# Kernel optimization log

Measured on AMD Instinct MI355X. Metric: run time of the kernel, lower is better.

Reference implementation:

```python
import jax, jax.numpy as jnp
import numpy as np

SOS_TOKEN = 0
VOCAB, EMBED, HIDDEN = 32000, 256, 256


def setup_inputs() -> dict:
    key = jax.random.key(0)
    ks = jax.random.split(key, 10)
    B, S, T = 32, 128, 128
    s = 0.05
    return {
        "encoder_outputs": jax.random.normal(ks[0], (B, S, HIDDEN), jnp.float32),
        "encoder_hidden": jax.random.normal(ks[1], (1, B, HIDDEN), jnp.float32),
        "target_tensor": jax.random.randint(ks[2], (B, T), 0, VOCAB),
        "embedding": jax.random.normal(ks[3], (VOCAB, EMBED), jnp.float32) * s,
        "W_ih": jax.random.normal(ks[4], (3 * HIDDEN, EMBED + HIDDEN), jnp.float32) * s,
        "W_hh": jax.random.normal(ks[5], (3 * HIDDEN, HIDDEN), jnp.float32) * s,
        "b_ih": jax.random.normal(ks[6], (3 * HIDDEN,), jnp.float32) * s,
        "b_hh": jax.random.normal(ks[7], (3 * HIDDEN,), jnp.float32) * s,
        "W_out": jax.random.normal(ks[8], (VOCAB, HIDDEN), jnp.float32) * s,
        "b_out": jax.random.normal(ks[9], (VOCAB,), jnp.float32) * s,
    }


def _decode(encoder_outputs, encoder_hidden, target_tensor, embedding,
            W_ih, W_hh, b_ih, b_hh, W_out, b_out):
    B, T = target_tensor.shape
    # full teacher forcing: decoder input at step t is target[t-1], step 0 is SOS
    dec_in = jnp.concatenate(
        [jnp.full((B, 1), SOS_TOKEN, dtype=target_tensor.dtype), target_tensor[:, :-1]], axis=1)
    emb = embedding[dec_in]                                     # (B,T,E)
    # attention: query = embedded input, key = value = encoder_outputs
    scores = jnp.einsum("bte,bse->bts", emb, encoder_outputs)   # (B,T,S)
    attn = jax.nn.softmax(scores, axis=2)
    context = jnp.einsum("bts,bsh->bth", attn, encoder_outputs)  # (B,T,H)
    x_seq = jnp.concatenate([emb, context], axis=2)             # (B,T,E+H)
    x_seq = jnp.swapaxes(x_seq, 0, 1)                           # (T,B,E+H)

    def gru_step(h, x):
        gi = x @ W_ih.T + b_ih                                  # (B,3H)
        gh = h @ W_hh.T + b_hh
        i_r, i_z, i_n = jnp.split(gi, 3, axis=1)
        h_r, h_z, h_n = jnp.split(gh, 3, axis=1)
        r = jax.nn.sigmoid(i_r + h_r)
        z = jax.nn.sigmoid(i_z + h_z)
        n = jnp.tanh(i_n + r * h_n)
        h_new = (1.0 - z) * n + z * h
        return h_new, h_new

    h0 = encoder_hidden[0]                                      # (B,H)
    _, hs = jax.lax.scan(gru_step, h0, x_seq)                   # (T,B,H)
    logits = hs @ W_out.T + b_out                               # (T,B,V)
    return jnp.swapaxes(logits, 0, 1)                           # (B,T,V)


def reference(encoder_outputs, encoder_hidden, target_tensor, embedding,
              W_ih, W_hh, b_ih, b_hh, W_out, b_out):
    return _decode(encoder_outputs, encoder_hidden, target_tensor, embedding,
                   W_ih, W_hh, b_ih, b_hh, W_out, b_out)
```

## Files before the change

### kernel.cpp

```cpp
#include <hip/hip_runtime.h>
#include <hip/hip_bf16.h>
#include <stdint.h>

typedef float    f32x4  __attribute__((ext_vector_type(4)));
typedef __bf16   bf16x8 __attribute__((ext_vector_type(8)));
typedef _Float16 f16x8  __attribute__((ext_vector_type(8)));
typedef _Float16 h2v    __attribute__((ext_vector_type(2)));

#define B_ 32
#define S_ 128
#define T_ 128
#define H_ 256
#define E_ 256
#define V_ 32000

__device__ __forceinline__ void gll16(const void* g, void* l) {
  __builtin_amdgcn_global_load_lds(
      (const __attribute__((address_space(1))) uint32_t*)g,
      (__attribute__((address_space(3))) uint32_t*)l,
      16, 0, 0);
}

__device__ __forceinline__ uint32_t pack_pair(float a, float b) {
  unsigned short lo = __builtin_bit_cast(unsigned short, (_Float16)a);
  unsigned short hi = __builtin_bit_cast(unsigned short, (_Float16)b);
  return (uint32_t)lo | ((uint32_t)hi << 16);
}

__device__ __forceinline__ uint32_t pack_bf16(float a, float b) {
  return (uint32_t)__builtin_bit_cast(unsigned short, __float2bfloat16(a)) |
         ((uint32_t)__builtin_bit_cast(unsigned short, __float2bfloat16(b)) << 16);
}

__device__ __forceinline__ float dot2(uint32_t w, uint32_t h, float acc) {
#if __has_builtin(__builtin_amdgcn_fdot2)
  return __builtin_amdgcn_fdot2(__builtin_bit_cast(h2v, w),
                                __builtin_bit_cast(h2v, h), acc, false);
#else
  h2v wv = __builtin_bit_cast(h2v, w);
  h2v hv = __builtin_bit_cast(h2v, h);
  return acc + (float)wv.x * (float)hv.x + (float)wv.y * (float)hv.y;
#endif
}

__device__ __forceinline__ float sigmoid_fast(float x) {
  return __fdividef(1.f, 1.f + __expf(-x));
}
__device__ __forceinline__ float tanh_fast(float x) {
  float e = __expf(2.f * fabsf(x));
  float t = 1.f - __fdividef(2.f, e + 1.f);
  return copysignf(t, x);
}

__global__ __launch_bounds__(256) void prep_kernel(
    const float* __restrict__ Wout, uint32_t* __restrict__ woutb,
    const float* __restrict__ Wih,  uint32_t* __restrict__ wihh,
    const float* __restrict__ Whh,  uint32_t* __restrict__ Wp,
    const float* __restrict__ enc, const int* __restrict__ tgt,
    const float* __restrict__ embt, uint32_t* __restrict__ xh)
{
  __shared__ __align__(16) char smem[32896];
  int bid = blockIdx.x;
  int tid = threadIdx.x;

  if (bid < 4000) {
    int i = (bid * 256 + tid) * 8;
    float4 a = *(const float4*)(Wout + i);
    float4 b = *(const float4*)(Wout + i + 4);
    uint4 o;
    o.x = pack_bf16(a.x, a.y); o.y = pack_bf16(a.z, a.w);
    o.z = pack_bf16(b.x, b.y); o.w = pack_bf16(b.z, b.w);
    *(uint4*)(woutb + (i >> 1)) = o;
    return;
  }
  if (bid < 4384) {
    int i = ((bid - 4000) * 256 + tid) * 4;
    float4 v = *(const float4*)(Wih + i);
    uint2 p;
    p.x = pack_pair(v.x, v.y);
    p.y = pack_pair(v.z, v.w);
    *(uint2*)(wihh + (i >> 1)) = p;
    return;
  }
  if (bid < 4408) {
    float (*lds)[257] = (float(*)[257])smem;
    int j0 = (bid - 4384) * 32;
    #pragma unroll 4
    for (int i = 0; i < 32; ++i)
      lds[i][tid] = Whh[(size_t)(j0 + i) * 256 + tid];
    __syncthreads();
    #pragma unroll 4
    for (int i = 0; i < 16; ++i) {
      int e = i * 256 + tid;
      int k2 = e >> 5;
      int jj = e & 31;
      Wp[(size_t)k2 * 768 + j0 + jj] = pack_pair(lds[jj][2 * k2], lds[jj][2 * k2 + 1]);
    }
    return;
  }
  {
    int idx = bid - 4408;
    int b   = idx & 31;
    int tc  = idx >> 5;
    float* e_sh    = (float*)smem;
    float* attn_sh = e_sh + 256;
    float* red_sh  = attn_sh + 128;
    const float* encb = enc + (size_t)b * S_ * H_;

    for (int tt = 0; tt < 8; ++tt) {
      int t = tc * 8 + tt;
      int tok = (t == 0) ? 0 : tgt[b * T_ + t - 1];
      float ev = embt[(size_t)tok * E_ + tid];
      e_sh[tid] = ev;
      {
        float other = __shfl_xor(ev, 1);
        if (!(tid & 1))
          xh[(size_t)(t * B_ + b) * 256 + (tid >> 1)] = pack_pair(ev, other);
      }
      __syncthreads();

      float sc = 0.f;
      if (tid < 128) {
        const float* er = encb + tid * H_;
        #pragma unroll 8
        for (int k = 0; k < 256; k += 4) {
          float4 e4 = *(const float4*)(e_sh + k);
          float4 r4 = *(const float4*)(er + k);
          sc += e4.x * r4.x; sc += e4.y * r4.y; sc += e4.z * r4.z; sc += e4.w * r4.w;
        }
        float mx = sc;
        #pragma unroll
        for (int o = 32; o > 0; o >>= 1) mx = fmaxf(mx, __shfl_xor(mx, o, 64));
        if ((tid & 63) == 0) red_sh[tid >> 6] = mx;
      }
      __syncthreads();
      float gmax = fmaxf(red_sh[0], red_sh[1]);
      float p = 0.f;
      if (tid < 128) {
        p = __expf(sc - gmax);
        float s = p;
        #pragma unroll
        for (int o = 32; o > 0; o >>= 1) s += __shfl_xor(s, o, 64);
        if ((tid & 63) == 0) red_sh[2 + (tid >> 6)] = s;
      }
      __syncthreads();
      float tot = red_sh[2] + red_sh[3];
      if (tid < 128) attn_sh[tid] = p / tot;
      __syncthreads();

      float ctx = 0.f;
      #pragma unroll 4
      for (int s = 0; s < 128; ++s) ctx += attn_sh[s] * encb[s * H_ + tid];
      {
        float other = __shfl_xor(ctx, 1);
        if (!(tid & 1))
          xh[(size_t)(t * B_ + b) * 256 + 128 + (tid >> 1)] = pack_pair(ctx, other);
      }
      __syncthreads();
    }
  }
}

__global__ __launch_bounds__(256) void gi_gemm_f16(
    const _Float16* __restrict__ A,
    const _Float16* __restrict__ Bm,
    const float* __restrict__ bih,
    float* __restrict__ gi)
{
  __shared__ _Float16 sA[128 * 64];
  __shared__ _Float16 sB[128 * 64];
  int tid = threadIdx.x;
  int n0 = blockIdx.x * 128;
  int m0 = blockIdx.y * 128;
  int lane = tid & 63;
  int wave = tid >> 6;
  int wm = (wave >> 1) * 64;
  int wn = (wave & 1) * 64;
  int srow = tid >> 3;
  int sk   = (tid & 7) * 8;
  f32x4 acc[4][4] = {};

  for (int kt = 0; kt < 512; kt += 64) {
    #pragma unroll
    for (int it = 0; it < 4; ++it) {
      int row = it * 32 + srow;
      gll16(A  + (size_t)(m0 + row) * 512 + kt + sk, &sA[row * 64 + sk]);
      gll16(Bm + (size_t)(n0 + row) * 512 + kt + sk, &sB[row * 64 + sk]);
    }
    __syncthreads();
    #pragma unroll
    for (int kk = 0; kk < 2; ++kk) {
      f16x8 af[4], bfr[4];
      #pragma unroll
      for (int m = 0; m < 4; ++m)
        af[m] = *(const f16x8*)&sA[(wm + m * 16 + (lane & 15)) * 64 + kk * 32 + (lane >> 4) * 8];
      #pragma unroll
      for (int n = 0; n < 4; ++n)
        bfr[n] = *(const f16x8*)&sB[(wn + n * 16 + (lane & 15)) * 64 + kk * 32 + (lane >> 4) * 8];
      #pragma unroll
      for (int m = 0; m < 4; ++m)
        #pragma unroll
        for (int n = 0; n < 4; ++n)
          acc[m][n] = __builtin_amdgcn_mfma_f32_16x16x32_f16(af[m], bfr[n], acc[m][n], 0, 0, 0);
    }
    __syncthreads();
  }

  #pragma unroll
  for (int n = 0; n < 4; ++n) {
    int col = n0 + wn + n * 16 + (lane & 15);
    float bv = bih[col];
    #pragma unroll
    for (int m = 0; m < 4; ++m) {
      int rbase = m0 + wm + m * 16 + (lane >> 4) * 4;
      #pragma unroll
      for (int r = 0; r < 4; ++r)
        gi[(size_t)(rbase + r) * 768 + col] = acc[m][n][r] + bv;
    }
  }
}

__global__ __launch_bounds__(768) void gru_kernel(
    const float*    __restrict__ gi,
    const uint32_t* __restrict__ Wp,
    const float*    __restrict__ bhh,
    const float*    __restrict__ h0,
    __hip_bfloat16* __restrict__ hs)
{
  int b   = blockIdx.x;
  int tid = threadIdx.x;
  int role = tid >> 8;
  int j    = tid & 255;
  __shared__ __align__(16) uint32_t h2[128];
  __shared__ float r_sh[256];
  __shared__ float z_sh[256];

  uint32_t w[128];
  #pragma unroll
  for (int i = 0; i < 128; ++i) w[i] = Wp[(size_t)i * 768 + tid];
  float bj = bhh[tid];

  float hprev = 0.f;
  if (role == 2) {
    hprev = h0[b * 256 + j];
    float other = __shfl_xor(hprev, 1);
    if (!(j & 1)) h2[j >> 1] = pack_pair(hprev, other);
  }
  float gval = gi[(size_t)b * 768 + tid];
  __syncthreads();

  for (int t = 0; t < 128; ++t) {
    float gnext = 0.f;
    if (t < 127) gnext = gi[(size_t)((t + 1) * 32 + b) * 768 + tid];

    float a0 = 0.f, a1 = 0.f, a2 = 0.f, a3 = 0.f;
    float a4 = 0.f, a5 = 0.f, a6 = 0.f, a7 = 0.f;
    #pragma unroll
    for (int k8 = 0; k8 < 16; ++k8) {
      uint4 ha = *(const uint4*)&h2[k8 * 8];
      uint4 hb = *(const uint4*)&h2[k8 * 8 + 4];
      a0 = dot2(w[k8 * 8 + 0], ha.x, a0);
      a1 = dot2(w[k8 * 8 + 1], ha.y, a1);
      a2 = dot2(w[k8 * 8 + 2], ha.z, a2);
      a3 = dot2(w[k8 * 8 + 3], ha.w, a3);
      a4 = dot2(w[k8 * 8 + 4], hb.x, a4);
      a5 = dot2(w[k8 * 8 + 5], hb.y, a5);
      a6 = dot2(w[k8 * 8 + 6], hb.z, a6);
      a7 = dot2(w[k8 * 8 + 7], hb.w, a7);
    }
    float gh = ((a0 + a1) + (a2 + a3)) + ((a4 + a5) + (a6 + a7)) + bj;

    if (role == 0)      r_sh[j] = sigmoid_fast(gval + gh);
    else if (role == 1) z_sh[j] = sigmoid_fast(gval + gh);
    __syncthreads();

    if (role == 2) {
      float r = r_sh[j];
      float z = z_sh[j];
      float n = tanh_fast(gval + r * gh);
      float hn = (1.f - z) * n + z * hprev;
      hprev = hn;
      hs[(size_t)(t * 32 + b) * 256 + j] = __float2bfloat16(hn);
      float other = __shfl_xor(hn, 1);
      if (!(j & 1)) h2[j >> 1] = pack_pair(hn, other);
    }
    gval = gnext;
    __syncthreads();
  }
}

__global__ __launch_bounds__(512) void logits_gemm(
    const __hip_bfloat16* __restrict__ A,
    const __hip_bfloat16* __restrict__ Bm,
    const float* __restrict__ bout,
    float* __restrict__ out)
{
  __shared__ __hip_bfloat16 sA[128 * 64];
  __shared__ __hip_bfloat16 sB[256 * 64];
  int tid = threadIdx.x;
  int bid = blockIdx.x;
  int chunk = bid & 7;
  int local = bid >> 3;
  int m0 = (chunk * 4 + (local & 3)) * 128;
  int n0 = (local >> 2) * 256;
  int lane = tid & 63;
  int wave = tid >> 6;
  int wm = (wave >> 2) * 64;
  int wn = (wave & 3) * 64;
  int srow = tid >> 3;
  int sk   = (tid & 7) * 8;
  f32x4 acc[4][4] = {};

  for (int kt = 0; kt < 256; kt += 64) {
    #pragma unroll
    for (int it = 0; it < 2; ++it) {
      int row = it * 64 + srow;
      gll16(A + (size_t)(m0 + row) * 256 + kt + sk, &sA[row * 64 + sk]);
    }
    #pragma unroll
    for (int it = 0; it < 4; ++it) {
      int row = it * 64 + srow;
      gll16(Bm + (size_t)(n0 + row) * 256 + kt + sk, &sB[row * 64 + sk]);
    }
    __syncthreads();
    #pragma unroll
    for (int kk = 0; kk < 2; ++kk) {
      bf16x8 af[4], bfr[4];
      #pragma unroll
      for (int m = 0; m < 4; ++m)
        af[m] = *(const bf16x8*)&sA[(wm + m * 16 + (lane & 15)) * 64 + kk * 32 + (lane >> 4) * 8];
      #pragma unroll
      for (int n = 0; n < 4; ++n)
        bfr[n] = *(const bf16x8*)&sB[(wn + n * 16 + (lane & 15)) * 64 + kk * 32 + (lane >> 4) * 8];
      #pragma unroll
      for (int m = 0; m < 4; ++m)
        #pragma unroll
        for (int n = 0; n < 4; ++n)
          acc[m][n] = __builtin_amdgcn_mfma_f32_16x16x32_bf16(af[m], bfr[n], acc[m][n], 0, 0, 0);
    }
    __syncthreads();
  }

  #pragma unroll
  for (int n = 0; n < 4; ++n) {
    int col = n0 + wn + n * 16 + (lane & 15);
    float bv = bout[col];
    #pragma unroll
    for (int m = 0; m < 4; ++m) {
      int rbase = m0 + wm + m * 16 + (lane >> 4) * 4;
      #pragma unroll
      for (int r = 0; r < 4; ++r) {
        int row = rbase + r;
        int t  = row >> 5;
        int bb = row & 31;
        out[(size_t)(bb * 128 + t) * 32000 + col] = acc[m][n][r] + bv;
      }
    }
  }
}

extern "C" void kernel_launch(void* const* d_in, const int* in_sizes, int n_in,
                              void* d_out, int out_size, void* d_ws, size_t ws_size,
                              hipStream_t stream) {
  const float* enc  = (const float*)d_in[0];
  const float* ench = (const float*)d_in[1];
  const int*   tgt  = (const int*)d_in[2];
  const float* embt = (const float*)d_in[3];
  const float* Wih  = (const float*)d_in[4];
  const float* Whh  = (const float*)d_in[5];
  const float* bih  = (const float*)d_in[6];
  const float* bhh  = (const float*)d_in[7];
  const float* Wout = (const float*)d_in[8];
  const float* bout = (const float*)d_in[9];
  float* out = (float*)d_out;

  char* ws = (char*)d_ws;
  float*          gi    = (float*)(ws);
  __hip_bfloat16* hs    = (__hip_bfloat16*)(ws + 12582912);
  __hip_bfloat16* woutb = (__hip_bfloat16*)(ws + 14680064);
  uint32_t*       xh    = (uint32_t*)(ws + 31064064);
  uint32_t*       wihh  = (uint32_t*)(ws + 35258368);

  uint32_t* Wp = (uint32_t*)(out + ((size_t)out_size - 98304));

  prep_kernel<<<4920, 256, 0, stream>>>(Wout, (uint32_t*)woutb, Wih, wihh,
                                        Whh, Wp, enc, tgt, embt, xh);
  gi_gemm_f16<<<dim3(6, 32), 256, 0, stream>>>((const _Float16*)xh, (const _Float16*)wihh, bih, gi);
  gru_kernel<<<32, 768, 0, stream>>>(gi, Wp, bhh, ench, hs);
  logits_gemm<<<4000, 512, 0, stream>>>(hs, woutb, bout, out);
}
```

Measured before the change: 526.8 us.

## Fuse GRU recurrence with logits GEMM using per-chunk flags for overlap

Merges the GRU kernel and the logits GEMM into one launch. The first 32 blocks run the recurrence and publish hidden states with atomic stores, bumping a release flag every 4 timesteps. The remaining blocks spin on the flag for their 128-row chunk and then compute logits, so the output GEMM overlaps the serial recurrence instead of waiting for it to finish. The GEMM tile shrinks to 128x128 and uses 256 of the 768 launched threads. Swapping the MFMA operands lets the epilogue write each output row with 16-byte vector stores. In exchange it relies on the GRU blocks being resident before the spinning blocks, and the idle threads plus the large register footprint of the shared kernel may lower GEMM occupancy.

```diff
diff --git a/kernel.cpp b/kernel.cpp
--- a/kernel.cpp
+++ b/kernel.cpp
@@ -50,6 +50,10 @@
   float e = __expf(2.f * fabsf(x));
   float t = 1.f - __fdividef(2.f, e + 1.f);
   return copysignf(t, x);
+}
+
+__global__ __launch_bounds__(512) void zero_flags(uint32_t* flags) {
+  flags[threadIdx.x] = 0;
 }
 
 __global__ __launch_bounds__(256) void prep_kernel(
@@ -220,106 +224,130 @@
   }
 }
 
-__global__ __launch_bounds__(768) void gru_kernel(
+__global__ __launch_bounds__(768) void gru_logits(
     const float*    __restrict__ gi,
     const uint32_t* __restrict__ Wp,
     const float*    __restrict__ bhh,
     const float*    __restrict__ h0,
-    __hip_bfloat16* __restrict__ hs)
+    uint32_t*       __restrict__ hsu,
+    const __hip_bfloat16* __restrict__ Bm,
+    const float*    __restrict__ bout,
+    float*          __restrict__ out,
+    uint32_t*       __restrict__ flags)
 {
-  int b   = blockIdx.x;
-  int tid = threadIdx.x;
-  int role = tid >> 8;
-  int j    = tid & 255;
   __shared__ __align__(16) uint32_t h2[128];
   __shared__ float r_sh[256];
   __shared__ float z_sh[256];
-
-  uint32_t w[128];
-  #pragma unroll
-  for (int i = 0; i < 128; ++i) w[i] = Wp[(size_t)i * 768 + tid];
-  float bj = bhh[tid];
-
-  float hprev = 0.f;
-  if (role == 2) {
-    hprev = h0[b * 256 + j];
-    float other = __shfl_xor(hprev, 1);
-    if (!(j & 1)) h2[j >> 1] = pack_pair(hprev, other);
-  }
-  float gval = gi[(size_t)b * 768 + tid];
-  __syncthreads();
-
-  for (int t = 0; t < 128; ++t) {
-    float gnext = 0.f;
-    if (t < 127) gnext = gi[(size_t)((t + 1) * 32 + b) * 768 + tid];
-
-    float a0 = 0.f, a1 = 0.f, a2 = 0.f, a3 = 0.f;
-    float a4 = 0.f, a5 = 0.f, a6 = 0.f, a7 = 0.f;
-    #pragma unroll
-    for (int k8 = 0; k8 < 16; ++k8) {
-      uint4 ha = *(const uint4*)&h2[k8 * 8];
-      uint4 hb = *(const uint4*)&h2[k8 * 8 + 4];
-      a0 = dot2(w[k8 * 8 + 0], ha.x, a0);
-      a1 = dot2(w[k8 * 8 + 1], ha.y, a1);
-      a2 = dot2(w[k8 * 8 + 2], ha.z, a2);
-      a3 = dot2(w[k8 * 8 + 3], ha.w, a3);
-      a4 = dot2(w[k8 * 8 + 4], hb.x, a4);
-      a5 = dot2(w[k8 * 8 + 5], hb.y, a5);
-      a6 = dot2(w[k8 * 8 + 6], hb.z, a6);
-      a7 = dot2(w[k8 * 8 + 7], hb.w, a7);
-    }
-    float gh = ((a0 + a1) + (a2 + a3)) + ((a4 + a5) + (a6 + a7)) + bj;
-
-    if (role == 0)      r_sh[j] = sigmoid_fast(gval + gh);
-    else if (role == 1) z_sh[j] = sigmoid_fast(gval + gh);
-    __syncthreads();
-
+  __shared__ __align__(16) __hip_bfloat16 sA[128 * 64];
+  __shared__ __align__(16) __hip_bfloat16 sB[128 * 64];
+
+  int bid = blockIdx.x;
+  int tid = threadIdx.x;
+
+  if (bid < 32) {
+    int b    = bid;
+    int role = tid >> 8;
+    int j    = tid & 255;
+
+    uint32_t w[128];
+    #pragma unroll
+    for (int i = 0; i < 128; ++i) w[i] = Wp[(size_t)i * 768 + tid];
+    float bj = bhh[tid];
+
+    float hprev = 0.f;
     if (role == 2) {
-      float r = r_sh[j];
-      float z = z_sh[j];
-      float n = tanh_fast(gval + r * gh);
-      float hn = (1.f - z) * n + z * hprev;
-      hprev = hn;
-      hs[(size_t)(t * 32 + b) * 256 + j] = __float2bfloat16(hn);
-      float other = __shfl_xor(hn, 1);
-      if (!(j & 1)) h2[j >> 1] = pack_pair(hn, other);
-    }
-    gval = gnext;
-    __syncthreads();
-  }
-}
-
-__global__ __launch_bounds__(512) void logits_gemm(
-    const __hip_bfloat16* __restrict__ A,
-    const __hip_bfloat16* __restrict__ Bm,
-    const float* __restrict__ bout,
-    float* __restrict__ out)
-{
-  __shared__ __hip_bfloat16 sA[128 * 64];
-  __shared__ __hip_bfloat16 sB[256 * 64];
-  int tid = threadIdx.x;
-  int bid = blockIdx.x;
-  int chunk = bid & 7;
-  int local = bid >> 3;
-  int m0 = (chunk * 4 + (local & 3)) * 128;
-  int n0 = (local >> 2) * 256;
+      hprev = h0[b * 256 + j];
+      float other = __shfl_xor(hprev, 1);
+      if (!(j & 1)) h2[j >> 1] = pack_pair(hprev, other);
+    }
+    float gval = gi[(size_t)b * 768 + tid];
+    __syncthreads();
+
+    for (int t = 0; t < 128; ++t) {
+      float gnext = 0.f;
+      if (t < 127) gnext = gi[(size_t)((t + 1) * 32 + b) * 768 + tid];
+
+      float a0 = 0.f, a1 = 0.f, a2 = 0.f, a3 = 0.f;
+      float a4 = 0.f, a5 = 0.f, a6 = 0.f, a7 = 0.f;
+      #pragma unroll
+      for (int k8 = 0; k8 < 16; ++k8) {
+        uint4 ha = *(const uint4*)&h2[k8 * 8];
+        uint4 hb = *(const uint4*)&h2[k8 * 8 + 4];
+        a0 = dot2(w[k8 * 8 + 0], ha.x, a0);
+        a1 = dot2(w[k8 * 8 + 1], ha.y, a1);
+        a2 = dot2(w[k8 * 8 + 2], ha.z, a2);
+        a3 = dot2(w[k8 * 8 + 3], ha.w, a3);
+        a4 = dot2(w[k8 * 8 + 4], hb.x, a4);
+        a5 = dot2(w[k8 * 8 + 5], hb.y, a5);
+        a6 = dot2(w[k8 * 8 + 6], hb.z, a6);
+        a7 = dot2(w[k8 * 8 + 7], hb.w, a7);
+      }
+      float gh = ((a0 + a1) + (a2 + a3)) + ((a4 + a5) + (a6 + a7)) + bj;
+
+      if (role == 0)      r_sh[j] = sigmoid_fast(gval + gh);
+      else if (role == 1) z_sh[j] = sigmoid_fast(gval + gh);
+      __syncthreads();
+
+      if (role == 2) {
+        float r = r_sh[j];
+        float z = z_sh[j];
+        float n = tanh_fast(gval + r * gh);
+        float hn = (1.f - z) * n + z * hprev;
+        hprev = hn;
+        float other = __shfl_xor(hn, 1);
+        if (!(j & 1)) {
+          h2[j >> 1] = pack_pair(hn, other);
+          __hip_atomic_store(&hsu[(size_t)(t * 32 + b) * 128 + (j >> 1)],
+                             pack_bf16(hn, other),
+                             __ATOMIC_RELAXED, __HIP_MEMORY_SCOPE_AGENT);
+        }
+      }
+      gval = gnext;
+      __syncthreads();
+
+      if ((t & 3) == 3 && tid == 0)
+        __hip_atomic_fetch_add(&flags[(t >> 2) * 16], 1u,
+                               __ATOMIC_RELEASE, __HIP_MEMORY_SCOPE_AGENT);
+    }
+    return;
+  }
+
+  if (tid >= 256) return;
+  int bid2 = bid - 32;
+  int c  = bid2 / 250;
+  int nn = bid2 % 250;
+  int m0 = c * 128;
+  int n0 = nn * 128;
   int lane = tid & 63;
   int wave = tid >> 6;
-  int wm = (wave >> 2) * 64;
-  int wn = (wave & 3) * 64;
+  int wm = (wave >> 1) * 64;
+  int wn = (wave & 1) * 64;
   int srow = tid >> 3;
   int sk   = (tid & 7) * 8;
+
+  if (tid == 0) {
+    while (__hip_atomic_load(&flags[c * 16], __ATOMIC_ACQUIRE,
+                             __HIP_MEMORY_SCOPE_AGENT) < 32u)
+      __builtin_amdgcn_s_sleep(32);
+  }
+  __syncthreads();
+
+  uint32_t* sAu = (uint32_t*)sA;
   f32x4 acc[4][4] = {};
 
   for (int kt = 0; kt < 256; kt += 64) {
     #pragma unroll
-    for (int it = 0; it < 2; ++it) {
-      int row = it * 64 + srow;
-      gll16(A + (size_t)(m0 + row) * 256 + kt + sk, &sA[row * 64 + sk]);
+    for (int i = 0; i < 16; ++i) {
+      int e = i * 256 + tid;
+      int row = e >> 5;
+      int cu  = e & 31;
+      uint32_t v = __hip_atomic_load(&hsu[(size_t)(m0 + row) * 128 + (kt >> 1) + cu],
+                                     __ATOMIC_RELAXED, __HIP_MEMORY_SCOPE_AGENT);
+      sAu[row * 32 + cu] = v;
     }
     #pragma unroll
     for (int it = 0; it < 4; ++it) {
-      int row = it * 64 + srow;
+      int row = it * 32 + srow;
       gll16(Bm + (size_t)(n0 + row) * 256 + kt + sk, &sB[row * 64 + sk]);
     }
     __syncthreads();
@@ -336,25 +364,23 @@
       for (int m = 0; m < 4; ++m)
         #pragma unroll
         for (int n = 0; n < 4; ++n)
-          acc[m][n] = __builtin_amdgcn_mfma_f32_16x16x32_bf16(af[m], bfr[n], acc[m][n], 0, 0, 0);
+          acc[m][n] = __builtin_amdgcn_mfma_f32_16x16x32_bf16(bfr[n], af[m], acc[m][n], 0, 0, 0);
     }
     __syncthreads();
   }
 
   #pragma unroll
-  for (int n = 0; n < 4; ++n) {
-    int col = n0 + wn + n * 16 + (lane & 15);
-    float bv = bout[col];
-    #pragma unroll
-    for (int m = 0; m < 4; ++m) {
-      int rbase = m0 + wm + m * 16 + (lane >> 4) * 4;
-      #pragma unroll
-      for (int r = 0; r < 4; ++r) {
-        int row = rbase + r;
-        int t  = row >> 5;
-        int bb = row & 31;
-        out[(size_t)(bb * 128 + t) * 32000 + col] = acc[m][n][r] + bv;
-      }
+  for (int m = 0; m < 4; ++m) {
+    int row = m0 + wm + m * 16 + (lane & 15);
+    int t  = row >> 5;
+    int bb = row & 31;
+    float* orow = out + (size_t)(bb * 128 + t) * 32000;
+    #pragma unroll
+    for (int n = 0; n < 4; ++n) {
+      int col0 = n0 + wn + n * 16 + (lane >> 4) * 4;
+      f32x4 bv = *(const f32x4*)&bout[col0];
+      f32x4 v = acc[m][n] + bv;
+      *(f32x4*)&orow[col0] = v;
     }
   }
 }
@@ -376,16 +402,17 @@
 
   char* ws = (char*)d_ws;
   float*          gi    = (float*)(ws);
-  __hip_bfloat16* hs    = (__hip_bfloat16*)(ws + 12582912);
+  uint32_t*       hsu   = (uint32_t*)(ws + 12582912);
   __hip_bfloat16* woutb = (__hip_bfloat16*)(ws + 14680064);
   uint32_t*       xh    = (uint32_t*)(ws + 31064064);
   uint32_t*       wihh  = (uint32_t*)(ws + 35258368);
+  uint32_t*       flags = (uint32_t*)(ws + 36044800);
 
   uint32_t* Wp = (uint32_t*)(out + ((size_t)out_size - 98304));
 
+  zero_flags<<<1, 512, 0, stream>>>(flags);
   prep_kernel<<<4920, 256, 0, stream>>>(Wout, (uint32_t*)woutb, Wih, wihh,
                                         Whh, Wp, enc, tgt, embt, xh);
   gi_gemm_f16<<<dim3(6, 32), 256, 0, stream>>>((const _Float16*)xh, (const _Float16*)wihh, bih, gi);
-  gru_kernel<<<32, 768, 0, stream>>>(gi, Wp, bhh, ench, hs);
-  logits_gemm<<<4000, 512, 0, stream>>>(hs, woutb, bout, out);
-}
+  gru_logits<<<8032, 768, 0, stream>>>(gi, Wp, bhh, ench, hsu, woutb, bout, out, flags);
+}
```

Result: slower. 839.9 us (+59.4%).

## Shrink logits GEMM tiles, swizzle LDS, and store output as float4 rows

Applied to the files above, without the earlier changes.

Halves the N tile of the logits GEMM to 128 with 256-thread blocks, doubling the grid to 8000 blocks. It adds an XOR swizzle on the LDS layout to avoid bank conflicts on fragment reads. It also swaps the MFMA operand order so each lane holds four consecutive columns, which lets the epilogue write float4 vectors and load the bias as float4. The aim is to cut LDS conflicts and speed up the large output store, at the cost of more A-tile reloads per output element.

```diff
diff --git a/kernel.cpp b/kernel.cpp
--- a/kernel.cpp
+++ b/kernel.cpp
@@ -289,72 +289,72 @@
   }
 }
 
-__global__ __launch_bounds__(512) void logits_gemm(
+__global__ __launch_bounds__(256) void logits_gemm(
     const __hip_bfloat16* __restrict__ A,
     const __hip_bfloat16* __restrict__ Bm,
     const float* __restrict__ bout,
     float* __restrict__ out)
 {
   __shared__ __hip_bfloat16 sA[128 * 64];
-  __shared__ __hip_bfloat16 sB[256 * 64];
+  __shared__ __hip_bfloat16 sB[128 * 64];
   int tid = threadIdx.x;
   int bid = blockIdx.x;
   int chunk = bid & 7;
   int local = bid >> 3;
   int m0 = (chunk * 4 + (local & 3)) * 128;
-  int n0 = (local >> 2) * 256;
+  int n0 = (local >> 2) * 128;
   int lane = tid & 63;
   int wave = tid >> 6;
-  int wm = (wave >> 2) * 64;
-  int wn = (wave & 3) * 64;
+  int wm = (wave >> 1) * 64;
+  int wn = (wave & 1) * 64;
   int srow = tid >> 3;
-  int sk   = (tid & 7) * 8;
+  int schunk = tid & 7;
   f32x4 acc[4][4] = {};
 
   for (int kt = 0; kt < 256; kt += 64) {
     #pragma unroll
-    for (int it = 0; it < 2; ++it) {
-      int row = it * 64 + srow;
-      gll16(A + (size_t)(m0 + row) * 256 + kt + sk, &sA[row * 64 + sk]);
-    }
-    #pragma unroll
     for (int it = 0; it < 4; ++it) {
-      int row = it * 64 + srow;
-      gll16(Bm + (size_t)(n0 + row) * 256 + kt + sk, &sB[row * 64 + sk]);
+      int row = it * 32 + srow;
+      int gc = ((schunk ^ (row & 7)) * 8);
+      gll16(A  + (size_t)(m0 + row) * 256 + kt + gc, &sA[row * 64 + schunk * 8]);
+      gll16(Bm + (size_t)(n0 + row) * 256 + kt + gc, &sB[row * 64 + schunk * 8]);
     }
     __syncthreads();
     #pragma unroll
     for (int kk = 0; kk < 2; ++kk) {
       bf16x8 af[4], bfr[4];
       #pragma unroll
-      for (int m = 0; m < 4; ++m)
-        af[m] = *(const bf16x8*)&sA[(wm + m * 16 + (lane & 15)) * 64 + kk * 32 + (lane >> 4) * 8];
-      #pragma unroll
-      for (int n = 0; n < 4; ++n)
-        bfr[n] = *(const bf16x8*)&sB[(wn + n * 16 + (lane & 15)) * 64 + kk * 32 + (lane >> 4) * 8];
+      for (int m = 0; m < 4; ++m) {
+        int r = wm + m * 16 + (lane & 15);
+        int pc = ((kk * 4 + (lane >> 4)) ^ (r & 7)) * 8;
+        af[m] = *(const bf16x8*)&sA[r * 64 + pc];
+      }
+      #pragma unroll
+      for (int n = 0; n < 4; ++n) {
+        int r = wn + n * 16 + (lane & 15);
+        int pc = ((kk * 4 + (lane >> 4)) ^ (r & 7)) * 8;
+        bfr[n] = *(const bf16x8*)&sB[r * 64 + pc];
+      }
       #pragma unroll
       for (int m = 0; m < 4; ++m)
         #pragma unroll
         for (int n = 0; n < 4; ++n)
-          acc[m][n] = __builtin_amdgcn_mfma_f32_16x16x32_bf16(af[m], bfr[n], acc[m][n], 0, 0, 0);
+          acc[m][n] = __builtin_amdgcn_mfma_f32_16x16x32_bf16(bfr[n], af[m], acc[m][n], 0, 0, 0);
     }
     __syncthreads();
   }
 
   #pragma unroll
-  for (int n = 0; n < 4; ++n) {
-    int col = n0 + wn + n * 16 + (lane & 15);
-    float bv = bout[col];
-    #pragma unroll
-    for (int m = 0; m < 4; ++m) {
-      int rbase = m0 + wm + m * 16 + (lane >> 4) * 4;
-      #pragma unroll
-      for (int r = 0; r < 4; ++r) {
-        int row = rbase + r;
-        int t  = row >> 5;
-        int bb = row & 31;
-        out[(size_t)(bb * 128 + t) * 32000 + col] = acc[m][n][r] + bv;
-      }
+  for (int m = 0; m < 4; ++m) {
+    int row = m0 + wm + m * 16 + (lane & 15);
+    int t  = row >> 5;
+    int bb = row & 31;
+    float* orow = out + (size_t)(bb * 128 + t) * 32000;
+    #pragma unroll
+    for (int n = 0; n < 4; ++n) {
+      int col0 = n0 + wn + n * 16 + (lane >> 4) * 4;
+      f32x4 bv = *(const f32x4*)&bout[col0];
+      *(f32x4*)&orow[col0] = acc[m][n] + bv;
     }
   }
 }
@@ -387,5 +387,5 @@
                                         Whh, Wp, enc, tgt, embt, xh);
   gi_gemm_f16<<<dim3(6, 32), 256, 0, stream>>>((const _Float16*)xh, (const _Float16*)wihh, bih, gi);
   gru_kernel<<<32, 768, 0, stream>>>(gi, Wp, bhh, ench, hs);
-  logits_gemm<<<4000, 512, 0, stream>>>(hs, woutb, bout, out);
-}
+  logits_gemm<<<8000, 256, 0, stream>>>(hs, woutb, bout, out);
+}
```

Result: no change. 536.9 us (+1.9%).
